# Performance work log

Measured on AMD Instinct MI355X. Metric: run time of the kernel, lower is better.

The kernel has to match this reference:

```python
import jax, jax.numpy as jnp
import numpy as np

B, C, T = 2, 128, 25000
OUT_C = 128
N_NODES = B * T            # 50000, nodes after flatten
N_EDGES = 800000           # avg degree 16


def setup_inputs() -> dict:
    key = jax.random.key(0)
    k1, k2, k3 = jax.random.split(key, 3)
    x = jax.random.normal(k1, (B, C, T), dtype=jnp.float32)
    W = jax.random.normal(k2, (C, OUT_C), dtype=jnp.float32) * (1.0 / np.sqrt(C))
    bias = jnp.zeros((OUT_C,), dtype=jnp.float32)
    edge_index = jax.random.randint(k3, (2, N_EDGES), 0, N_NODES, dtype=jnp.int64)
    return {"x": x, "W": W, "bias": bias, "edge_index": edge_index}


def reference(x, W, bias, edge_index):
    b, c, t = x.shape
    n = b * t
    flat = x.transpose(0, 2, 1).reshape(n, c)          # [N, C]
    h = flat @ W                                       # [N, OUT_C] transform first (GCNConv)
    src, dst = edge_index[0], edge_index[1]
    # in-degree with self-loops (PyG GCNConv default symmetric norm)
    deg = jnp.zeros((n,), dtype=h.dtype).at[dst].add(1.0) + 1.0
    dinv_sqrt = jax.lax.rsqrt(deg)
    norm = dinv_sqrt[src] * dinv_sqrt[dst]             # [E]
    msgs = h[src] * norm[:, None]                      # [E, OUT_C] gather + scale
    agg = jax.ops.segment_sum(msgs, dst, num_segments=n)
    agg = agg + h * (1.0 / deg)[:, None]               # self-loop term: norm_ii = 1/deg_i
    out = jax.nn.relu(agg + bias)
    return out.reshape(b, t, -1).transpose(0, 2, 1)    # [B, OUT_C, T]
```

## Files before the change

### kernel.cpp

```cpp
#include <hip/hip_runtime.h>

#define TT 25000
#define BB 2
#define CC 128
#define NN (BB*TT)
#define NB ((NN + 255) / 256)
#define NBPAD 256
#define GEMMB ((NN + 63) / 64)

typedef __attribute__((ext_vector_type(8))) short bf16x8;
typedef __attribute__((ext_vector_type(4))) float f32x4;

__device__ inline unsigned short f2bf(float f) {
    unsigned int u = __float_as_uint(f);
    u += 0x7FFF + ((u >> 16) & 1);
    return (unsigned short)(u >> 16);
}
__device__ inline float bfhi(unsigned int v) { return __uint_as_float(v << 16); }
__device__ inline float bflo(unsigned int v) { return __uint_as_float(v & 0xFFFF0000u); }

__global__ __launch_bounds__(256) void k_deg(const int* __restrict__ dst, int E,
                                             int* __restrict__ deg,
                                             int* __restrict__ eseq,
                                             int* __restrict__ bsum) {
    __shared__ int hist[NB];
    for (int i = threadIdx.x; i < NB; i += 256) hist[i] = 0;
    __syncthreads();

    int base = blockIdx.x * 1024 + threadIdx.x;
    int d[4]; bool ok[4];
#pragma unroll
    for (int u = 0; u < 4; ++u) {
        int i = base + u * 256;
        ok[u] = (i < E);
        d[u] = ok[u] ? dst[i] : 0;
    }
#pragma unroll
    for (int u = 0; u < 4; ++u)
        if (ok[u]) {
            eseq[base + u * 256] = atomicAdd(&deg[d[u]], 1);
            atomicAdd(&hist[d[u] >> 8], 1);
        }
    __syncthreads();
    for (int i = threadIdx.x; i < NB; i += 256) {
        int v = hist[i];
        if (v) atomicAdd(&bsum[i], v);
    }
}

__global__ __launch_bounds__(256) void k_scan2(const int* __restrict__ deg,
                                               const int* __restrict__ bsum,
                                               int* __restrict__ off,
                                               float* __restrict__ dinv) {
    __shared__ int part[256];
    __shared__ int bpref;
    int tid = threadIdx.x;
    int i = blockIdx.x * 256 + tid;

    part[tid] = (tid < NB && tid < blockIdx.x) ? bsum[tid] : 0;
    __syncthreads();
#pragma unroll
    for (int o = 128; o > 0; o >>= 1) {
        if (tid < o) part[tid] += part[tid + o];
        __syncthreads();
    }
    if (tid == 0) bpref = part[0];
    __syncthreads();
    int base = bpref;
    __syncthreads();

    int v = (i < NN) ? deg[i] : 0;
    part[tid] = v;
    __syncthreads();
#pragma unroll
    for (int o = 1; o < 256; o <<= 1) {
        int u = (tid >= o) ? part[tid - o] : 0;
        __syncthreads();
        part[tid] += u;
        __syncthreads();
    }
    int incl = part[tid];
    if (i < NN) {
        off[i]  = base + incl - v;
        dinv[i] = rsqrtf((float)(v + 1));
    }
    if (i == NN - 1) off[NN] = base + incl;
}

__global__ __launch_bounds__(256) void k_fg(const float* __restrict__ x,
                                            const float* __restrict__ W,
                                            const float* __restrict__ dinv,
                                            unsigned short* __restrict__ h,
                                            const int* __restrict__ src,
                                            const int* __restrict__ dst, int E,
                                            const int* __restrict__ off,
                                            const int* __restrict__ eseq,
                                            int* __restrict__ csr_src) {
    __shared__ __align__(16) unsigned short a_lds[4][4][64][8];
    __shared__ __align__(16) unsigned short b_lds[8][4][64][8];
    int bx = blockIdx.x;
    if (bx >= GEMMB) {
        int i = (bx - GEMMB) * 256 + threadIdx.x;
        if (i < E) {
            int d = dst[i];
            csr_src[off[d] + eseq[i]] = src[i];
        }
        return;
    }

    int tid = threadIdx.x;
    int n0 = bx * 64;

    {
        int m = tid & 63;
        int n = n0 + m;
        bool ok = (n < NN);
        int b = 0, t = 0;
        if (ok) { b = n / TT; t = n - b * TT; }
        const float* xp = x + ((size_t)b * CC) * TT + t;
        int mt = m >> 4, lm = m & 15;
#pragma unroll
        for (int p = 0; p < 4; ++p) {
            int kg = (tid >> 6) + p * 4;
            unsigned short tmp[8];
#pragma unroll
            for (int j = 0; j < 8; ++j) {
                float v = ok ? xp[(size_t)(kg * 8 + j) * TT] : 0.f;
                tmp[j] = f2bf(v);
            }
            int kk = kg >> 2, q = kg & 3;
            *(bf16x8*)&a_lds[mt][kk][lm | (q << 4)][0] = *(bf16x8*)tmp;
        }
    }
    {
        int nc = tid & 127;
        int nt = nc >> 4, ln = nc & 15;
#pragma unroll
        for (int p = 0; p < 8; ++p) {
            int kg = (tid >> 7) + p * 2;
            unsigned short tmp[8];
#pragma unroll
            for (int j = 0; j < 8; ++j)
                tmp[j] = f2bf(W[(kg * 8 + j) * CC + nc]);
            int kk = kg >> 2, q = kg & 3;
            *(bf16x8*)&b_lds[nt][kk][ln | (q << 4)][0] = *(bf16x8*)tmp;
        }
    }
    __syncthreads();

    int lane = tid & 63;
    int w = tid >> 6;
    f32x4 acc[8];
#pragma unroll
    for (int nt = 0; nt < 8; ++nt) acc[nt] = (f32x4){0.f, 0.f, 0.f, 0.f};
#pragma unroll
    for (int kk = 0; kk < 4; ++kk) {
        bf16x8 a = *(const bf16x8*)&a_lds[w][kk][lane][0];
#pragma unroll
        for (int nt = 0; nt < 8; ++nt) {
            bf16x8 bb = *(const bf16x8*)&b_lds[nt][kk][lane][0];
            acc[nt] = __builtin_amdgcn_mfma_f32_16x16x32_bf16(a, bb, acc[nt], 0, 0, 0);
        }
    }

    int q = lane >> 4, col = lane & 15;
    int nodebase = n0 + w * 16 + q * 4;
    float di[4];
#pragma unroll
    for (int r = 0; r < 4; ++r) {
        int nn = nodebase + r;
        di[r] = (nn < NN) ? dinv[nn] : 0.f;
    }
#pragma unroll
    for (int nt = 0; nt < 8; ++nt) {
#pragma unroll
        for (int r = 0; r < 4; ++r) {
            int nn = nodebase + r;
            if (nn < NN)
                h[(size_t)nn * CC + nt * 16 + col] = f2bf(di[r] * acc[nt][r]);
        }
    }
}

__global__ __launch_bounds__(512) void k_aggt(const unsigned int* __restrict__ hb,
                                              const int* __restrict__ off,
                                              const int* __restrict__ csr_src,
                                              const float* __restrict__ dinv,
                                              const float* __restrict__ bias,
                                              float* __restrict__ out) {
    __shared__ float tile[32][129];
    int lane = threadIdx.x & 63;
    int w    = threadIdx.x >> 6;
    int n0   = blockIdx.x * 32;
    const float2 bb = ((const float2*)bias)[lane];

#pragma unroll
    for (int r = 0; r < 4; ++r) {
        int lt = w * 4 + r;
        int n = n0 + lt;
        if (n < NN) {
            float ax = 0.f, ay = 0.f;
            int e0 = off[n], e1 = off[n + 1];

            for (int c0 = e0; c0 < e1; c0 += 64) {
                int cnt = e1 - c0; if (cnt > 64) cnt = 64;
                int li = lane < cnt ? lane : cnt - 1;
                int iv = csr_src[c0 + li];
                int j = 0;
                for (; j + 16 <= cnt; j += 16) {
                    int s[16];
#pragma unroll
                    for (int u = 0; u < 16; ++u) s[u] = __shfl(iv, j + u, 64);
                    unsigned int v[16];
#pragma unroll
                    for (int u = 0; u < 16; ++u) v[u] = hb[(size_t)s[u] * 64 + lane];
#pragma unroll
                    for (int u = 0; u < 16; ++u) { ax += bfhi(v[u]); ay += bflo(v[u]); }
                }
                for (; j + 4 <= cnt; j += 4) {
                    int s[4];
#pragma unroll
                    for (int u = 0; u < 4; ++u) s[u] = __shfl(iv, j + u, 64);
                    unsigned int v[4];
#pragma unroll
                    for (int u = 0; u < 4; ++u) v[u] = hb[(size_t)s[u] * 64 + lane];
#pragma unroll
                    for (int u = 0; u < 4; ++u) { ax += bfhi(v[u]); ay += bflo(v[u]); }
                }
                for (; j < cnt; ++j) {
                    int s = __shfl(iv, j, 64);
                    unsigned int v = hb[(size_t)s * 64 + lane];
                    ax += bfhi(v); ay += bflo(v);
                }
            }

            unsigned int hv = hb[(size_t)n * 64 + lane];
            ax += bfhi(hv);
            ay += bflo(hv);
            float di = dinv[n];
            float rx = fmaxf(fmaf(di, ax, bb.x), 0.f);
            float ry = fmaxf(fmaf(di, ay, bb.y), 0.f);
            tile[lt][2 * lane]     = rx;
            tile[lt][2 * lane + 1] = ry;
        }
    }
    __syncthreads();

    int tx = threadIdx.x & 31;
    int cg = threadIdx.x >> 5;
    int n = n0 + tx;
    if (n < NN) {
        int b = n / TT, t = n - b * TT;
#pragma unroll
        for (int i = 0; i < 8; ++i) {
            int ch = cg + i * 16;
            out[((size_t)b * CC + ch) * TT + t] = tile[tx][ch];
        }
    }
}

extern "C" void kernel_launch(void* const* d_in, const int* in_sizes, int n_in,
                              void* d_out, int out_size, void* d_ws, size_t ws_size,
                              hipStream_t stream) {
    const float* x    = (const float*)d_in[0];
    const float* W    = (const float*)d_in[1];
    const float* bias = (const float*)d_in[2];
    const int*   ei   = (const int*)d_in[3];
    int E = in_sizes[3] / 2;
    const int* src = ei;
    const int* dst = ei + E;
    float* out = (float*)d_out;

    char* ws = (char*)d_ws;
    size_t o = 0;
    unsigned short* h = (unsigned short*)(ws + o); o += (size_t)NN * CC * 2;
    int*   deg  = (int*)  (ws + o); o += (size_t)NN * 4;
    int*   bsum = (int*)  (ws + o); o += (size_t)NBPAD * 4;
    float* dinv = (float*)(ws + o); o += (size_t)NN * 4;
    int*   off  = (int*)  (ws + o); o += (size_t)(NN + 1) * 4 + 12;
    int*   eseq = (int*)  (ws + o); o += (size_t)E * 4;
    int*   csrs = (int*)  (ws + o); o += (size_t)E * 4;

    hipMemsetAsync(deg, 0, (size_t)(NN + NBPAD) * 4, stream);

    int fb = (E + 255) / 256;
    k_deg  <<<(E + 1023) / 1024, 256, 0, stream>>>(dst, E, deg, eseq, bsum);
    k_scan2<<<NB, 256, 0, stream>>>(deg, bsum, off, dinv);
    k_fg   <<<GEMMB + fb, 256, 0, stream>>>(x, W, dinv, h, src, dst, E, off, eseq, csrs);
    k_aggt <<<(NN + 31) / 32, 512, 0, stream>>>((const unsigned int*)h, off, csrs, dinv, bias, out);
}
```

Baseline: 195.6 us.

## Overlap node GEMM with degree counting and move source-side normalization into aggregation

The dense transform no longer depends on the degree scan, so it runs in the same launch as the atomic degree counting. GEMM blocks and degree blocks are interleaved by block parity, which lets the compute-heavy and atomic-heavy work share the GPU. To allow this, h is stored unscaled, and the aggregation kernel gathers dinv[src] per edge and applies it with an FMA. The CSR fill becomes its own kernel and stores source indices as 16-bit values, which halves index traffic but only works because the node count is below 65536. The trade-off is an extra scattered dinv load per edge in the gather loop.

```diff
diff --git a/kernel.cpp b/kernel.cpp
--- a/kernel.cpp
+++ b/kernel.cpp
@@ -19,32 +19,107 @@
 __device__ inline float bfhi(unsigned int v) { return __uint_as_float(v << 16); }
 __device__ inline float bflo(unsigned int v) { return __uint_as_float(v & 0xFFFF0000u); }
 
-__global__ __launch_bounds__(256) void k_deg(const int* __restrict__ dst, int E,
-                                             int* __restrict__ deg,
-                                             int* __restrict__ eseq,
-                                             int* __restrict__ bsum) {
+__global__ __launch_bounds__(256) void k_dg(const float* __restrict__ x,
+                                            const float* __restrict__ W,
+                                            unsigned short* __restrict__ h,
+                                            const int* __restrict__ dst, int E,
+                                            int* __restrict__ deg,
+                                            int* __restrict__ eseq,
+                                            int* __restrict__ bsum) {
+    __shared__ __align__(16) unsigned short a_lds[4][4][64][8];
+    __shared__ __align__(16) unsigned short b_lds[8][4][64][8];
     __shared__ int hist[NB];
-    for (int i = threadIdx.x; i < NB; i += 256) hist[i] = 0;
-    __syncthreads();
-
-    int base = blockIdx.x * 1024 + threadIdx.x;
-    int d[4]; bool ok[4];
-#pragma unroll
-    for (int u = 0; u < 4; ++u) {
-        int i = base + u * 256;
-        ok[u] = (i < E);
-        d[u] = ok[u] ? dst[i] : 0;
-    }
-#pragma unroll
-    for (int u = 0; u < 4; ++u)
-        if (ok[u]) {
-            eseq[base + u * 256] = atomicAdd(&deg[d[u]], 1);
-            atomicAdd(&hist[d[u] >> 8], 1);
-        }
-    __syncthreads();
-    for (int i = threadIdx.x; i < NB; i += 256) {
-        int v = hist[i];
-        if (v) atomicAdd(&bsum[i], v);
+    int idx = blockIdx.x >> 1;
+    int tid = threadIdx.x;
+
+    if (blockIdx.x & 1) {
+        int db = (E + 1023) >> 10;
+        if (idx >= db) return;
+        for (int i = tid; i < NB; i += 256) hist[i] = 0;
+        __syncthreads();
+        int base = idx * 1024 + tid;
+#pragma unroll
+        for (int u = 0; u < 4; ++u) {
+            int i = base + u * 256;
+            if (i < E) {
+                int d = dst[i];
+                eseq[i] = atomicAdd(&deg[d], 1);
+                atomicAdd(&hist[d >> 8], 1);
+            }
+        }
+        __syncthreads();
+        for (int i = tid; i < NB; i += 256) {
+            int v = hist[i];
+            if (v) atomicAdd(&bsum[i], v);
+        }
+        return;
+    }
+
+    if (idx >= GEMMB) return;
+    int n0 = idx * 64;
+
+    {
+        int m = tid & 63;
+        int n = n0 + m;
+        bool ok = (n < NN);
+        int b = 0, t = 0;
+        if (ok) { b = n / TT; t = n - b * TT; }
+        const float* xp = x + ((size_t)b * CC) * TT + t;
+        int mt = m >> 4, lm = m & 15;
+#pragma unroll
+        for (int p = 0; p < 4; ++p) {
+            int kg = (tid >> 6) + p * 4;
+            unsigned short tmp[8];
+#pragma unroll
+            for (int j = 0; j < 8; ++j) {
+                float v = ok ? xp[(size_t)(kg * 8 + j) * TT] : 0.f;
+                tmp[j] = f2bf(v);
+            }
+            int kk = kg >> 2, q = kg & 3;
+            *(bf16x8*)&a_lds[mt][kk][lm | (q << 4)][0] = *(bf16x8*)tmp;
+        }
+    }
+    {
+        int nc = tid & 127;
+        int nt = nc >> 4, ln = nc & 15;
+#pragma unroll
+        for (int p = 0; p < 8; ++p) {
+            int kg = (tid >> 7) + p * 2;
+            unsigned short tmp[8];
+#pragma unroll
+            for (int j = 0; j < 8; ++j)
+                tmp[j] = f2bf(W[(kg * 8 + j) * CC + nc]);
+            int kk = kg >> 2, q = kg & 3;
+            *(bf16x8*)&b_lds[nt][kk][ln | (q << 4)][0] = *(bf16x8*)tmp;
+        }
+    }
+    __syncthreads();
+
+    int lane = tid & 63;
+    int w = tid >> 6;
+    f32x4 acc[8];
+#pragma unroll
+    for (int nt = 0; nt < 8; ++nt) acc[nt] = (f32x4){0.f, 0.f, 0.f, 0.f};
+#pragma unroll
+    for (int kk = 0; kk < 4; ++kk) {
+        bf16x8 a = *(const bf16x8*)&a_lds[w][kk][lane][0];
+#pragma unroll
+        for (int nt = 0; nt < 8; ++nt) {
+            bf16x8 bb = *(const bf16x8*)&b_lds[nt][kk][lane][0];
+            acc[nt] = __builtin_amdgcn_mfma_f32_16x16x32_bf16(a, bb, acc[nt], 0, 0, 0);
+        }
+    }
+
+    int q = lane >> 4, col = lane & 15;
+    int nodebase = n0 + w * 16 + q * 4;
+#pragma unroll
+    for (int nt = 0; nt < 8; ++nt) {
+#pragma unroll
+        for (int r = 0; r < 4; ++r) {
+            int nn = nodebase + r;
+            if (nn < NN)
+                h[(size_t)nn * CC + nt * 16 + col] = f2bf(acc[nt][r]);
+        }
     }
 }
 
@@ -87,104 +162,21 @@
     if (i == NN - 1) off[NN] = base + incl;
 }
 
-__global__ __launch_bounds__(256) void k_fg(const float* __restrict__ x,
-                                            const float* __restrict__ W,
-                                            const float* __restrict__ dinv,
-                                            unsigned short* __restrict__ h,
-                                            const int* __restrict__ src,
-                                            const int* __restrict__ dst, int E,
-                                            const int* __restrict__ off,
-                                            const int* __restrict__ eseq,
-                                            int* __restrict__ csr_src) {
-    __shared__ __align__(16) unsigned short a_lds[4][4][64][8];
-    __shared__ __align__(16) unsigned short b_lds[8][4][64][8];
-    int bx = blockIdx.x;
-    if (bx >= GEMMB) {
-        int i = (bx - GEMMB) * 256 + threadIdx.x;
-        if (i < E) {
-            int d = dst[i];
-            csr_src[off[d] + eseq[i]] = src[i];
-        }
-        return;
-    }
-
-    int tid = threadIdx.x;
-    int n0 = bx * 64;
-
-    {
-        int m = tid & 63;
-        int n = n0 + m;
-        bool ok = (n < NN);
-        int b = 0, t = 0;
-        if (ok) { b = n / TT; t = n - b * TT; }
-        const float* xp = x + ((size_t)b * CC) * TT + t;
-        int mt = m >> 4, lm = m & 15;
-#pragma unroll
-        for (int p = 0; p < 4; ++p) {
-            int kg = (tid >> 6) + p * 4;
-            unsigned short tmp[8];
-#pragma unroll
-            for (int j = 0; j < 8; ++j) {
-                float v = ok ? xp[(size_t)(kg * 8 + j) * TT] : 0.f;
-                tmp[j] = f2bf(v);
-            }
-            int kk = kg >> 2, q = kg & 3;
-            *(bf16x8*)&a_lds[mt][kk][lm | (q << 4)][0] = *(bf16x8*)tmp;
-        }
-    }
-    {
-        int nc = tid & 127;
-        int nt = nc >> 4, ln = nc & 15;
-#pragma unroll
-        for (int p = 0; p < 8; ++p) {
-            int kg = (tid >> 7) + p * 2;
-            unsigned short tmp[8];
-#pragma unroll
-            for (int j = 0; j < 8; ++j)
-                tmp[j] = f2bf(W[(kg * 8 + j) * CC + nc]);
-            int kk = kg >> 2, q = kg & 3;
-            *(bf16x8*)&b_lds[nt][kk][ln | (q << 4)][0] = *(bf16x8*)tmp;
-        }
-    }
-    __syncthreads();
-
-    int lane = tid & 63;
-    int w = tid >> 6;
-    f32x4 acc[8];
-#pragma unroll
-    for (int nt = 0; nt < 8; ++nt) acc[nt] = (f32x4){0.f, 0.f, 0.f, 0.f};
-#pragma unroll
-    for (int kk = 0; kk < 4; ++kk) {
-        bf16x8 a = *(const bf16x8*)&a_lds[w][kk][lane][0];
-#pragma unroll
-        for (int nt = 0; nt < 8; ++nt) {
-            bf16x8 bb = *(const bf16x8*)&b_lds[nt][kk][lane][0];
-            acc[nt] = __builtin_amdgcn_mfma_f32_16x16x32_bf16(a, bb, acc[nt], 0, 0, 0);
-        }
-    }
-
-    int q = lane >> 4, col = lane & 15;
-    int nodebase = n0 + w * 16 + q * 4;
-    float di[4];
-#pragma unroll
-    for (int r = 0; r < 4; ++r) {
-        int nn = nodebase + r;
-        di[r] = (nn < NN) ? dinv[nn] : 0.f;
-    }
-#pragma unroll
-    for (int nt = 0; nt < 8; ++nt) {
-#pragma unroll
-        for (int r = 0; r < 4; ++r) {
-            int nn = nodebase + r;
-            if (nn < NN)
-                h[(size_t)nn * CC + nt * 16 + col] = f2bf(di[r] * acc[nt][r]);
-        }
+__global__ __launch_bounds__(256) void k_fill(const int* __restrict__ src,
+                                              const int* __restrict__ dst, int E,
+                                              const int* __restrict__ off,
+                                              const int* __restrict__ eseq,
+                                              unsigned short* __restrict__ csr_src) {
+    int i = blockIdx.x * blockDim.x + threadIdx.x;
+    if (i < E) {
+        int d = dst[i];
+        csr_src[off[d] + eseq[i]] = (unsigned short)src[i];
     }
 }
 
 __global__ __launch_bounds__(512) void k_aggt(const unsigned int* __restrict__ hb,
                                               const int* __restrict__ off,
-                                              const int* __restrict__ csr_src,
+                                              const unsigned short* __restrict__ csr_src,
                                               const float* __restrict__ dinv,
                                               const float* __restrict__ bias,
                                               float* __restrict__ out) {
@@ -205,7 +197,7 @@
             for (int c0 = e0; c0 < e1; c0 += 64) {
                 int cnt = e1 - c0; if (cnt > 64) cnt = 64;
                 int li = lane < cnt ? lane : cnt - 1;
-                int iv = csr_src[c0 + li];
+                int iv = (int)csr_src[c0 + li];
                 int j = 0;
                 for (; j + 16 <= cnt; j += 16) {
                     int s[16];
@@ -214,8 +206,14 @@
                     unsigned int v[16];
 #pragma unroll
                     for (int u = 0; u < 16; ++u) v[u] = hb[(size_t)s[u] * 64 + lane];
-#pragma unroll
-                    for (int u = 0; u < 16; ++u) { ax += bfhi(v[u]); ay += bflo(v[u]); }
+                    float dv[16];
+#pragma unroll
+                    for (int u = 0; u < 16; ++u) dv[u] = dinv[s[u]];
+#pragma unroll
+                    for (int u = 0; u < 16; ++u) {
+                        ax = fmaf(dv[u], bfhi(v[u]), ax);
+                        ay = fmaf(dv[u], bflo(v[u]), ay);
+                    }
                 }
                 for (; j + 4 <= cnt; j += 4) {
                     int s[4];
@@ -224,22 +222,30 @@
                     unsigned int v[4];
 #pragma unroll
                     for (int u = 0; u < 4; ++u) v[u] = hb[(size_t)s[u] * 64 + lane];
-#pragma unroll
-                    for (int u = 0; u < 4; ++u) { ax += bfhi(v[u]); ay += bflo(v[u]); }
+                    float dv[4];
+#pragma unroll
+                    for (int u = 0; u < 4; ++u) dv[u] = dinv[s[u]];
+#pragma unroll
+                    for (int u = 0; u < 4; ++u) {
+                        ax = fmaf(dv[u], bfhi(v[u]), ax);
+                        ay = fmaf(dv[u], bflo(v[u]), ay);
+                    }
                 }
                 for (; j < cnt; ++j) {
                     int s = __shfl(iv, j, 64);
                     unsigned int v = hb[(size_t)s * 64 + lane];
-                    ax += bfhi(v); ay += bflo(v);
+                    float dv = dinv[s];
+                    ax = fmaf(dv, bfhi(v), ax);
+                    ay = fmaf(dv, bflo(v), ay);
                 }
             }
 
             unsigned int hv = hb[(size_t)n * 64 + lane];
-            ax += bfhi(hv);
-            ay += bflo(hv);
-            float di = dinv[n];
-            float rx = fmaxf(fmaf(di, ax, bb.x), 0.f);
-            float ry = fmaxf(fmaf(di, ay, bb.y), 0.f);
+            float dn = dinv[n];
+            ax = fmaf(dn, bfhi(hv), ax);
+            ay = fmaf(dn, bflo(hv), ay);
+            float rx = fmaxf(fmaf(dn, ax, bb.x), 0.f);
+            float ry = fmaxf(fmaf(dn, ay, bb.y), 0.f);
             tile[lt][2 * lane]     = rx;
             tile[lt][2 * lane + 1] = ry;
         }
@@ -279,13 +285,14 @@
     float* dinv = (float*)(ws + o); o += (size_t)NN * 4;
     int*   off  = (int*)  (ws + o); o += (size_t)(NN + 1) * 4 + 12;
     int*   eseq = (int*)  (ws + o); o += (size_t)E * 4;
-    int*   csrs = (int*)  (ws + o); o += (size_t)E * 4;
+    unsigned short* csrs = (unsigned short*)(ws + o); o += (size_t)E * 2;
 
     hipMemsetAsync(deg, 0, (size_t)(NN + NBPAD) * 4, stream);
 
-    int fb = (E + 255) / 256;
-    k_deg  <<<(E + 1023) / 1024, 256, 0, stream>>>(dst, E, deg, eseq, bsum);
+    int db = (E + 1023) / 1024;
+    int mx = (GEMMB > db) ? GEMMB : db;
+    k_dg   <<<2 * mx, 256, 0, stream>>>(x, W, h, dst, E, deg, eseq, bsum);
     k_scan2<<<NB, 256, 0, stream>>>(deg, bsum, off, dinv);
-    k_fg   <<<GEMMB + fb, 256, 0, stream>>>(x, W, dinv, h, src, dst, E, off, eseq, csrs);
+    k_fill <<<(E + 255) / 256, 256, 0, stream>>>(src, dst, E, off, eseq, csrs);
     k_aggt <<<(NN + 31) / 32, 512, 0, stream>>>((const unsigned int*)h, off, csrs, dinv, bias, out);
 }
```

New measurement: 182.8 us. 6.6% less time.
